# Performance work log

Measured on AMD Instinct MI355X. Metric: run time of the kernel, lower is better.

The kernel has to match this reference:

```python
import jax, jax.numpy as jnp
import numpy as np

B, S, E, H = 256, 512, 256, 256
START = 0
MASK_VAL = -100000.0


def _u(k, shape, s):
    return jax.random.uniform(k, shape, jnp.float32, -s, s)


def setup_inputs() -> dict:
    key = jax.random.key(0)
    ks = jax.random.split(key, 14)
    se = 1.0 / np.sqrt(E)
    sh = 1.0 / np.sqrt(H)
    return {
        'inputs': jax.random.uniform(ks[0], (B, S, 2), jnp.float32),
        'W_embed': _u(ks[1], (2, E), se),
        'enc_Wih': _u(ks[2], (4 * H, E), sh),
        'enc_Whh': _u(ks[3], (4 * H, H), sh),
        'enc_bih': _u(ks[4], (4 * H,), sh),
        'enc_bhh': _u(ks[5], (4 * H,), sh),
        'dec_Wih': _u(ks[6], (4 * H, E), sh),
        'dec_Whh': _u(ks[7], (4 * H, H), sh),
        'dec_bih': _u(ks[8], (4 * H,), sh),
        'dec_bhh': _u(ks[9], (4 * H,), sh),
        'Wq': _u(ks[10], (H, H), sh),
        'Wref': _u(ks[11], (H, H), sh),
        'v': _u(ks[12], (H,), sh),
    }


def lstm_cell(x, h, c, Wih, Whh, bih, bhh):
    # PyTorch gate order: input, forget, cell(g), output
    gates = x @ Wih.T + h @ Whh.T + bih + bhh
    i, f, g, o = jnp.split(gates, 4, axis=-1)
    c = jax.nn.sigmoid(f) * c + jax.nn.sigmoid(i) * jnp.tanh(g)
    h = jax.nn.sigmoid(o) * jnp.tanh(c)
    return h, c


def reference(inputs, W_embed, enc_Wih, enc_Whh, enc_bih, enc_bhh,
              dec_Wih, dec_Whh, dec_bih, dec_bhh, Wq, Wref, v):
    # GraphEmbedding: per-node linear projection of 2-D coords -> [B,S,E]
    emb = jnp.einsum('bsi,ie->bse', inputs, W_embed)

    # Encoder LSTM over the sequence
    def enc_step(carry, x):
        h, c = carry
        h, c = lstm_cell(x, h, c, enc_Wih, enc_Whh, enc_bih, enc_bhh)
        return (h, c), h

    h0 = jnp.zeros((B, H), emb.dtype)
    c0 = jnp.zeros((B, H), emb.dtype)
    (h, c), enc_out = jax.lax.scan(enc_step, (h0, c0), jnp.swapaxes(emb, 0, 1))
    enc_out = jnp.swapaxes(enc_out, 0, 1)  # [B,S,H]

    # Pointer attention: precompute W_ref projection of encoder outputs
    ref_proj = enc_out @ Wref.T  # [B,S,H]

    mask0 = jnp.zeros((B, S), bool).at[:, START].set(True)
    dec_in0 = emb[:, START, :]
    batch_ix = jnp.arange(B)

    def dec_step(carry, key):
        h, c, x, mask = carry
        h, c = lstm_cell(x, h, c, dec_Wih, dec_Whh, dec_bih, dec_bhh)
        q = (h @ Wq.T)[:, None, :]                            # [B,1,H]
        logits = jnp.einsum('bsh,h->bs', jnp.tanh(q + ref_proj), v)
        logits = jnp.where(mask, MASK_VAL, logits)
        chosen = jax.random.categorical(key, logits)          # [B]
        logp = jax.nn.log_softmax(logits, axis=-1)
        lp = jnp.take_along_axis(logp, chosen[:, None], axis=1)[:, 0]
        mask = mask.at[batch_ix, chosen].set(True)
        x = emb[batch_ix, chosen]
        return (h, c, x, mask), (lp, chosen)

    keys = jax.random.split(jax.random.key(1), S - 1)
    _, (lps, idxs) = jax.lax.scan(dec_step, (h, c, dec_in0, mask0), keys)

    logprobs = jnp.swapaxes(lps, 0, 1)                        # [B,S-1]
    start_col = jnp.full((B, 1), START, dtype=idxs.dtype)
    indices = jnp.concatenate([start_col, jnp.swapaxes(idxs, 0, 1)], axis=1)  # [B,S]
    return logprobs, indices
```

## Files before the change

kernel.cpp:

```cpp
#include <hip/hip_runtime.h>
#include <stdint.h>
#include <math.h>

#define Bn 256
#define Sn 512
#define En 256
#define Hn 256
#define Gn 1024
#define NSTEP 511
#define MASK_VAL -100000.0

#define PARTITIONABLE 1

__device__ __forceinline__ uint32_t rotl32(uint32_t v, int d) {
  return (v << d) | (v >> (32 - d));
}

__device__ __forceinline__ void threefry2x32(uint32_t k0, uint32_t k1,
                                             uint32_t x0, uint32_t x1,
                                             uint32_t& o0, uint32_t& o1) {
  const uint32_t ks2 = k0 ^ k1 ^ 0x1BD11BDAu;
  x0 += k0; x1 += k1;
  x0 += x1; x1 = rotl32(x1, 13); x1 ^= x0;
  x0 += x1; x1 = rotl32(x1, 15); x1 ^= x0;
  x0 += x1; x1 = rotl32(x1, 26); x1 ^= x0;
  x0 += x1; x1 = rotl32(x1,  6); x1 ^= x0;
  x0 += k1; x1 += ks2 + 1u;
  x0 += x1; x1 = rotl32(x1, 17); x1 ^= x0;
  x0 += x1; x1 = rotl32(x1, 29); x1 ^= x0;
  x0 += x1; x1 = rotl32(x1, 16); x1 ^= x0;
  x0 += x1; x1 = rotl32(x1, 24); x1 ^= x0;
  x0 += ks2; x1 += k0 + 2u;
  x0 += x1; x1 = rotl32(x1, 13); x1 ^= x0;
  x0 += x1; x1 = rotl32(x1, 15); x1 ^= x0;
  x0 += x1; x1 = rotl32(x1, 26); x1 ^= x0;
  x0 += x1; x1 = rotl32(x1,  6); x1 ^= x0;
  x0 += k0; x1 += k1 + 3u;
  x0 += x1; x1 = rotl32(x1, 17); x1 ^= x0;
  x0 += x1; x1 = rotl32(x1, 29); x1 ^= x0;
  x0 += x1; x1 = rotl32(x1, 16); x1 ^= x0;
  x0 += x1; x1 = rotl32(x1, 24); x1 ^= x0;
  x0 += k1; x1 += ks2 + 4u;
  x0 += x1; x1 = rotl32(x1, 13); x1 ^= x0;
  x0 += x1; x1 = rotl32(x1, 15); x1 ^= x0;
  x0 += x1; x1 = rotl32(x1, 26); x1 ^= x0;
  x0 += x1; x1 = rotl32(x1,  6); x1 ^= x0;
  x0 += ks2; x1 += k0 + 5u;
  o0 = x0; o1 = x1;
}

__device__ __forceinline__ uint32_t random_word(uint32_t k0, uint32_t k1, uint32_t n) {
#if PARTITIONABLE
  uint32_t o0, o1;
  threefry2x32(k0, k1, 0u, n, o0, o1);
  return o0 ^ o1;
#else
  const uint32_t half = (Bn * Sn) / 2;
  uint32_t lane = (n < half) ? n : (n - half);
  uint32_t o0, o1;
  threefry2x32(k0, k1, lane, lane + half, o0, o1);
  return (n < half) ? o0 : o1;
#endif
}

__device__ __forceinline__ double sigmoid64(double x) {
  return 1.0 / (1.0 + exp(-x));
}

__global__ __launch_bounds__(256) void k_wihe(const float* __restrict__ wemb,
                                              const float* __restrict__ wih,
                                              const float* __restrict__ bih,
                                              const float* __restrict__ bhh,
                                              double* __restrict__ wihe,
                                              double* __restrict__ bias) {
  int j = blockIdx.x * blockDim.x + threadIdx.x;
  if (j >= Gn) return;
  double a0 = 0.0, a1 = 0.0;
  for (int e = 0; e < En; ++e) {
    double w = (double)wih[j * En + e];
    a0 += (double)wemb[e] * w;
    a1 += (double)wemb[En + e] * w;
  }
  wihe[j] = a0;
  wihe[Gn + j] = a1;
  bias[j] = (double)bih[j] + (double)bhh[j];
}

__global__ __launch_bounds__(256) void k_keys(uint32_t* __restrict__ keys) {
  int j = blockIdx.x * blockDim.x + threadIdx.x;
  if (j >= NSTEP) return;
#if PARTITIONABLE
  uint32_t o0, o1;
  threefry2x32(0u, 1u, 0u, (uint32_t)j, o0, o1);
  keys[2 * j] = o0; keys[2 * j + 1] = o1;
#else
  uint32_t w[2];
  #pragma unroll
  for (int q = 0; q < 2; ++q) {
    uint32_t m = (uint32_t)(2 * j + q);
    uint32_t lane = (m < NSTEP) ? m : (m - NSTEP);
    uint32_t o0, o1;
    threefry2x32(0u, 1u, lane, lane + NSTEP, o0, o1);
    w[q] = (m < NSTEP) ? o0 : o1;
  }
  keys[2 * j] = w[0]; keys[2 * j + 1] = w[1];
#endif
}

__global__ __launch_bounds__(256) void k_t32(const float* __restrict__ src,
                                             float* __restrict__ dst) {
  int idx = blockIdx.x * blockDim.x + threadIdx.x;
  int k = idx >> 8, j = idx & 255;
  dst[idx] = src[j * Hn + k];
}

__global__ __launch_bounds__(256) void k_t32w(const float* __restrict__ src,
                                              float* __restrict__ dst) {
  int idx = blockIdx.x * blockDim.x + threadIdx.x;
  int k = idx >> 10, j = idx & 1023;
  dst[idx] = src[j * Hn + k];
}

__global__ __launch_bounds__(256) void k_init(float* __restrict__ out) {
  int idx = blockIdx.x * blockDim.x + threadIdx.x;
  if (idx < Bn) out[Bn * NSTEP + idx * Sn] = 0.0f;
}

struct AttnS {
  double qpart[4][256];
  double p2[2][512];
  double sg[2][512];
  float2 qv2[256];
};

__global__ __launch_bounds__(1024, 4) void k_main(
    const float* __restrict__ inp,
    const double* __restrict__ wihe_e, const double* __restrict__ bias_e,
    const float* __restrict__ whhT_e,
    const double* __restrict__ wihe_d, const double* __restrict__ bias_d,
    const float* __restrict__ whhT_d,
    const float* __restrict__ wrefT, const float* __restrict__ wqT,
    const float* __restrict__ v,
    float* __restrict__ refT,
    const uint32_t* __restrict__ keys,
    float* __restrict__ out) {
  __shared__ __align__(16) double sh_h[Hn];
  __shared__ double sh_g[Gn];
  __shared__ AttnS at;

  const int b   = blockIdx.x;
  const int tid = threadIdx.x;
  const int w   = tid >> 6;
  const int l   = tid & 63;
  const int gsel = tid >> 8;

  const double bj_e = bias_e[tid], w0e = wihe_e[tid], w1e = wihe_e[Gn + tid];
  const double bj_d = bias_d[tid], w0d = wihe_d[tid], w1d = wihe_d[Gn + tid];
  const float vreg = (tid < Hn) ? v[tid] : 0.0f;

  double creg = 0.0;
  if (tid < Hn) sh_h[tid] = 0.0;
  __syncthreads();

  const float* wcol_e = whhT_e + tid;
  const float* wcol_d = whhT_d + tid;
  const int part = tid >> 8, tcol = tid & 255;

  for (int s = 0; s < Sn; ++s) {
    {
      double x0 = (double)inp[((size_t)b * Sn + s) * 2 + 0];
      double x1 = (double)inp[((size_t)b * Sn + s) * 2 + 1];
      double acc = bj_e + x0 * w0e + x1 * w1e;
      #pragma unroll 4
      for (int k = 0; k < Hn; k += 2) {
        double2 hv = *(const double2*)&sh_h[k];
        acc += hv.x * (double)wcol_e[(size_t)k << 10];
        acc += hv.y * (double)wcol_e[(size_t)(k + 1) << 10];
      }
      sh_g[tid] = (gsel == 2) ? tanh(acc) : sigmoid64(acc);
    }
    __syncthreads();
    if (tid < Hn) {
      double ti = sh_g[tid];
      double tf = sh_g[256 + tid];
      double tg = sh_g[512 + tid];
      double to = sh_g[768 + tid];
      double cn = tf * creg + ti * tg;
      double hn = to * tanh(cn);
      creg = cn;
      sh_h[tid] = hn;
    }
    __syncthreads();
    {
      double racc = 0.0;
      #pragma unroll 8
      for (int i = 0; i < 64; ++i) {
        int k = part * 64 + i;
        racc += sh_h[k] * (double)wrefT[(size_t)k * Hn + tcol];
      }
      at.qpart[part][tcol] = racc;
    }
    __syncthreads();
    if (tid < Hn) {
      double r = (at.qpart[0][tid] + at.qpart[1][tid]) +
                 (at.qpart[2][tid] + at.qpart[3][tid]);
      refT[((size_t)b * Hn + tid) * Sn + s] = (float)r;
    }
  }

  int ch = 0;
  unsigned mbits = (l == 0) ? 1u : 0u;
  for (int t = 0; t < NSTEP; ++t) {
    const int par = t & 1;
    {
      int col = __builtin_amdgcn_readfirstlane(ch);
      double x0 = (double)inp[((size_t)b * Sn + col) * 2 + 0];
      double x1 = (double)inp[((size_t)b * Sn + col) * 2 + 1];
      double acc = bj_d + x0 * w0d + x1 * w1d;
      #pragma unroll 4
      for (int k = 0; k < Hn; k += 2) {
        double2 hv = *(const double2*)&sh_h[k];
        acc += hv.x * (double)wcol_d[(size_t)k << 10];
        acc += hv.y * (double)wcol_d[(size_t)(k + 1) << 10];
      }
      sh_g[tid] = (gsel == 2) ? tanh(acc) : sigmoid64(acc);
    }
    __syncthreads();
    if (tid < Hn) {
      double ti = sh_g[tid];
      double tf = sh_g[256 + tid];
      double tg = sh_g[512 + tid];
      double to = sh_g[768 + tid];
      double cn = tf * creg + ti * tg;
      double hn = to * tanh(cn);
      creg = cn;
      sh_h[tid] = hn;
    } else if (tid >= 512) {
      const uint32_t k0 = keys[2 * t], k1 = keys[2 * t + 1];
      int s0 = tid - 512;
      uint32_t wrd = random_word(k0, k1, (uint32_t)(b * Sn + s0));
      float uf = __uint_as_float((wrd >> 9) | 0x3f800000u) - 1.0f;
      uf = fmaxf(uf, 1.17549435e-38f);
      at.sg[par][s0] = -log(-log((double)uf));
    }
    __syncthreads();
    {
      double qa = 0.0;
      #pragma unroll 8
      for (int i = 0; i < 64; ++i) {
        int k = part * 64 + i;
        qa += sh_h[k] * (double)wqT[(size_t)k * Hn + tcol];
      }
      at.qpart[part][tcol] = qa;
    }
    __syncthreads();
    if (tid < Hn) {
      double q = (at.qpart[0][tid] + at.qpart[1][tid]) +
                 (at.qpart[2][tid] + at.qpart[3][tid]);
      at.qv2[tid] = make_float2((float)q, vreg);
    }
    __syncthreads();
    {
      const int sE = tid & 511, ph = tid >> 9;
      const float* rT = refT + ((size_t)b * Hn + ph * 128) * Sn + sE;
      double la = 0.0;
      for (int c = 0; c < 16; ++c) {
        float st[8];
        #pragma unroll
        for (int i = 0; i < 8; ++i)
          st[i] = rT[(size_t)(c * 8 + i) * Sn];
        #pragma unroll
        for (int i = 0; i < 8; ++i) {
          int t2 = ph * 128 + c * 8 + i;
          float2 qv = at.qv2[t2];
          la += (double)qv.y * (double)tanhf(qv.x + st[i]);
        }
      }
      at.p2[ph][sE] = la;
    }
    __syncthreads();
    double slv[8];
    {
      #pragma unroll
      for (int k = 0; k < 8; ++k) {
        int s2 = l + k * 64;
        slv[k] = (mbits >> k) & 1u ? (double)MASK_VAL
                                   : (at.p2[0][s2] + at.p2[1][s2]);
      }
      double bz = slv[0] + at.sg[par][l];
      int bi = l;
      #pragma unroll
      for (int k = 1; k < 8; ++k) {
        int s2 = l + k * 64;
        double z2 = slv[k] + at.sg[par][s2];
        if (z2 > bz || (z2 == bz && s2 < bi)) { bz = z2; bi = s2; }
      }
      #pragma unroll
      for (int m = 32; m >= 1; m >>= 1) {
        double oz = __shfl_xor(bz, m);
        int    oi = __shfl_xor(bi, m);
        if (oz > bz || (oz == bz && oi < bi)) { bz = oz; bi = oi; }
      }
      ch = bi;
    }
    if (w == 1) {
      double bm = slv[0];
      #pragma unroll
      for (int k = 1; k < 8; ++k) bm = fmax(bm, slv[k]);
      #pragma unroll
      for (int m = 32; m >= 1; m >>= 1) bm = fmax(bm, __shfl_xor(bm, m));
      double ps = 0.0;
      #pragma unroll
      for (int k = 0; k < 8; ++k) ps += exp(slv[k] - bm);
      #pragma unroll
      for (int m = 32; m >= 1; m >>= 1) ps += __shfl_xor(ps, m);
      if (l == 0) {
        double lse = bm + log(ps);
        double slch = at.p2[0][ch] + at.p2[1][ch];
        double lp = slch - lse;
        out[(size_t)b * NSTEP + t] = (float)lp;
        out[(size_t)Bn * NSTEP + (size_t)b * Sn + (t + 1)] = (float)ch;
      }
    }
    if ((ch & 63) == l) mbits |= 1u << (ch >> 6);
  }
}

extern "C" void kernel_launch(void* const* d_in, const int* in_sizes, int n_in,
                              void* d_out, int out_size, void* d_ws, size_t ws_size,
                              hipStream_t stream) {
  const float* inp  = (const float*)d_in[0];
  const float* wemb = (const float*)d_in[1];
  const float* eWih = (const float*)d_in[2];
  const float* eWhh = (const float*)d_in[3];
  const float* ebih = (const float*)d_in[4];
  const float* ebhh = (const float*)d_in[5];
  const float* dWih = (const float*)d_in[6];
  const float* dWhh = (const float*)d_in[7];
  const float* dbih = (const float*)d_in[8];
  const float* dbhh = (const float*)d_in[9];
  const float* Wq   = (const float*)d_in[10];
  const float* Wref = (const float*)d_in[11];
  const float* v    = (const float*)d_in[12];
  float* out = (float*)d_out;

  char* ws = (char*)d_ws;
  size_t off = 0;
  auto alloc = [&](size_t bytes) -> void* {
    void* p = (void*)(ws + off);
    off += (bytes + 255) & ~(size_t)255;
    return p;
  };
  float*    refT   = (float*)   alloc((size_t)Bn * Sn * Hn * sizeof(float));
  float*    whhT_e = (float*)   alloc((size_t)Hn * Gn * sizeof(float));
  float*    whhT_d = (float*)   alloc((size_t)Hn * Gn * sizeof(float));
  float*    wqT    = (float*)   alloc((size_t)Hn * Hn * sizeof(float));
  float*    wrefT  = (float*)   alloc((size_t)Hn * Hn * sizeof(float));
  double*   wihe_e = (double*)  alloc(2 * Gn * sizeof(double));
  double*   wihe_d = (double*)  alloc(2 * Gn * sizeof(double));
  double*   bias_e = (double*)  alloc(Gn * sizeof(double));
  double*   bias_d = (double*)  alloc(Gn * sizeof(double));
  uint32_t* keys   = (uint32_t*)alloc(2 * NSTEP * sizeof(uint32_t));
  (void)ws_size; (void)in_sizes; (void)n_in; (void)out_size;

  k_wihe<<<Gn / 256, 256, 0, stream>>>(wemb, eWih, ebih, ebhh, wihe_e, bias_e);
  k_wihe<<<Gn / 256, 256, 0, stream>>>(wemb, dWih, dbih, dbhh, wihe_d, bias_d);
  k_keys<<<2, 256, 0, stream>>>(keys);
  k_t32<<<(Hn * Hn) / 256, 256, 0, stream>>>(Wq, wqT);
  k_t32<<<(Hn * Hn) / 256, 256, 0, stream>>>(Wref, wrefT);
  k_t32w<<<(Hn * Gn) / 256, 256, 0, stream>>>(eWhh, whhT_e);
  k_t32w<<<(Hn * Gn) / 256, 256, 0, stream>>>(dWhh, whhT_d);
  k_init<<<1, 256, 0, stream>>>(out);

  k_main<<<Bn, 1024, 0, stream>>>(
      inp, wihe_e, bias_e, whhT_e, wihe_d, bias_d, whhT_d,
      wrefT, wqT, v, refT, keys, out);
}
```

Before: 27.30 ms.

## Pack recurrent weights as float4 along k and double-buffer refT loads

Recurrent weight matrices are repacked so that each thread loads four consecutive k values with one float4 load, replacing four scalar strided loads in both the encoder and decoder gate matvecs. The attention logit loop also now issues two batches of eight refT loads before consuming them, which raises memory-level parallelism. The cost is more registers per thread, which could hurt the 1024-thread blocks at four waves per SIMD, plus a different packing kernel.

```diff
diff --git a/kernel.cpp b/kernel.cpp
--- a/kernel.cpp
+++ b/kernel.cpp
@@ -114,11 +114,11 @@
   dst[idx] = src[j * Hn + k];
 }
 
-__global__ __launch_bounds__(256) void k_t32w(const float* __restrict__ src,
-                                              float* __restrict__ dst) {
-  int idx = blockIdx.x * blockDim.x + threadIdx.x;
-  int k = idx >> 10, j = idx & 1023;
-  dst[idx] = src[j * Hn + k];
+__global__ __launch_bounds__(256) void k_pack_whh(const float* __restrict__ src,
+                                                  float* __restrict__ dst) {
+  int o = blockIdx.x * 256 + threadIdx.x;
+  int r = o & 3, j = (o >> 2) & 1023, k4 = o >> 12;
+  dst[o] = src[j * Hn + k4 * 4 + r];
 }
 
 __global__ __launch_bounds__(256) void k_init(float* __restrict__ out) {
@@ -136,9 +136,9 @@
 __global__ __launch_bounds__(1024, 4) void k_main(
     const float* __restrict__ inp,
     const double* __restrict__ wihe_e, const double* __restrict__ bias_e,
-    const float* __restrict__ whhT_e,
+    const float* __restrict__ whh2_e,
     const double* __restrict__ wihe_d, const double* __restrict__ bias_d,
-    const float* __restrict__ whhT_d,
+    const float* __restrict__ whh2_d,
     const float* __restrict__ wrefT, const float* __restrict__ wqT,
     const float* __restrict__ v,
     float* __restrict__ refT,
@@ -162,8 +162,8 @@
   if (tid < Hn) sh_h[tid] = 0.0;
   __syncthreads();
 
-  const float* wcol_e = whhT_e + tid;
-  const float* wcol_d = whhT_d + tid;
+  const float4* w4e = (const float4*)whh2_e + tid;
+  const float4* w4d = (const float4*)whh2_d + tid;
   const int part = tid >> 8, tcol = tid & 255;
 
   for (int s = 0; s < Sn; ++s) {
@@ -172,10 +172,14 @@
       double x1 = (double)inp[((size_t)b * Sn + s) * 2 + 1];
       double acc = bj_e + x0 * w0e + x1 * w1e;
       #pragma unroll 4
-      for (int k = 0; k < Hn; k += 2) {
-        double2 hv = *(const double2*)&sh_h[k];
-        acc += hv.x * (double)wcol_e[(size_t)k << 10];
-        acc += hv.y * (double)wcol_e[(size_t)(k + 1) << 10];
+      for (int k4 = 0; k4 < 64; ++k4) {
+        float4 wv = w4e[(size_t)k4 << 10];
+        double2 h0 = *(const double2*)&sh_h[4 * k4];
+        double2 h1 = *(const double2*)&sh_h[4 * k4 + 2];
+        acc += h0.x * (double)wv.x;
+        acc += h0.y * (double)wv.y;
+        acc += h1.x * (double)wv.z;
+        acc += h1.y * (double)wv.w;
       }
       sh_g[tid] = (gsel == 2) ? tanh(acc) : sigmoid64(acc);
     }
@@ -218,10 +222,14 @@
       double x1 = (double)inp[((size_t)b * Sn + col) * 2 + 1];
       double acc = bj_d + x0 * w0d + x1 * w1d;
       #pragma unroll 4
-      for (int k = 0; k < Hn; k += 2) {
-        double2 hv = *(const double2*)&sh_h[k];
-        acc += hv.x * (double)wcol_d[(size_t)k << 10];
-        acc += hv.y * (double)wcol_d[(size_t)(k + 1) << 10];
+      for (int k4 = 0; k4 < 64; ++k4) {
+        float4 wv = w4d[(size_t)k4 << 10];
+        double2 h0 = *(const double2*)&sh_h[4 * k4];
+        double2 h1 = *(const double2*)&sh_h[4 * k4 + 2];
+        acc += h0.x * (double)wv.x;
+        acc += h0.y * (double)wv.y;
+        acc += h1.x * (double)wv.z;
+        acc += h1.y * (double)wv.w;
       }
       sh_g[tid] = (gsel == 2) ? tanh(acc) : sigmoid64(acc);
     }
@@ -264,16 +272,25 @@
       const int sE = tid & 511, ph = tid >> 9;
       const float* rT = refT + ((size_t)b * Hn + ph * 128) * Sn + sE;
       double la = 0.0;
-      for (int c = 0; c < 16; ++c) {
-        float st[8];
+      for (int c = 0; c < 16; c += 2) {
+        float stA[8], stB[8];
         #pragma unroll
         for (int i = 0; i < 8; ++i)
-          st[i] = rT[(size_t)(c * 8 + i) * Sn];
+          stA[i] = rT[(size_t)(c * 8 + i) * Sn];
+        #pragma unroll
+        for (int i = 0; i < 8; ++i)
+          stB[i] = rT[(size_t)((c + 1) * 8 + i) * Sn];
         #pragma unroll
         for (int i = 0; i < 8; ++i) {
           int t2 = ph * 128 + c * 8 + i;
           float2 qv = at.qv2[t2];
-          la += (double)qv.y * (double)tanhf(qv.x + st[i]);
+          la += (double)qv.y * (double)tanhf(qv.x + stA[i]);
+        }
+        #pragma unroll
+        for (int i = 0; i < 8; ++i) {
+          int t2 = ph * 128 + (c + 1) * 8 + i;
+          float2 qv = at.qv2[t2];
+          la += (double)qv.y * (double)tanhf(qv.x + stB[i]);
         }
       }
       at.p2[ph][sE] = la;
@@ -352,8 +369,8 @@
     return p;
   };
   float*    refT   = (float*)   alloc((size_t)Bn * Sn * Hn * sizeof(float));
-  float*    whhT_e = (float*)   alloc((size_t)Hn * Gn * sizeof(float));
-  float*    whhT_d = (float*)   alloc((size_t)Hn * Gn * sizeof(float));
+  float*    whh2_e = (float*)   alloc((size_t)Hn * Gn * sizeof(float));
+  float*    whh2_d = (float*)   alloc((size_t)Hn * Gn * sizeof(float));
   float*    wqT    = (float*)   alloc((size_t)Hn * Hn * sizeof(float));
   float*    wrefT  = (float*)   alloc((size_t)Hn * Hn * sizeof(float));
   double*   wihe_e = (double*)  alloc(2 * Gn * sizeof(double));
@@ -368,11 +385,11 @@
   k_keys<<<2, 256, 0, stream>>>(keys);
   k_t32<<<(Hn * Hn) / 256, 256, 0, stream>>>(Wq, wqT);
   k_t32<<<(Hn * Hn) / 256, 256, 0, stream>>>(Wref, wrefT);
-  k_t32w<<<(Hn * Gn) / 256, 256, 0, stream>>>(eWhh, whhT_e);
-  k_t32w<<<(Hn * Gn) / 256, 256, 0, stream>>>(dWhh, whhT_d);
+  k_pack_whh<<<(Hn * Gn) / 256, 256, 0, stream>>>(eWhh, whh2_e);
+  k_pack_whh<<<(Hn * Gn) / 256, 256, 0, stream>>>(dWhh, whh2_d);
   k_init<<<1, 256, 0, stream>>>(out);
 
   k_main<<<Bn, 1024, 0, stream>>>(
-      inp, wihe_e, bias_e, whhT_e, wihe_d, bias_d, whhT_d,
+      inp, wihe_e, bias_e, whh2_e, wihe_d, bias_d, whh2_d,
       wrefT, wqT, v, refT, keys, out);
 }
```

Result: slower. 35.77 ms (+31.0%).
